# Optimization experiments

Hardware: AMD Instinct MI355X
Metric: run time of the kernel (lower is better)

Reference implementation:

```python
import jax, jax.numpy as jnp
import numpy as np
import math

B_, T_, C_ = 4, 1024, 1024
N_HEAD = 16
INT_D = 64
ALPHA = 1.000001  # sparsity_alpha
N_ITER = 50       # entmax_bisect default iteration count


def _entmax_bisect_impl(X):
    # alpha-entmax over last axis via bisection (entmax package algorithm)
    d = X.shape[-1]
    power = 1.0 / (ALPHA - 1.0)
    Xa = X * (ALPHA - 1.0)
    max_val = jnp.max(Xa, axis=-1, keepdims=True)
    tau_lo = max_val - 1.0                      # gp(1) = 1**power
    tau_hi = max_val - (1.0 / d) ** power       # gp(1/d)
    dm = tau_hi - tau_lo
    p0 = jnp.power(jnp.maximum(Xa - tau_lo, 0.0), power)

    def body(i, carry):
        tau_lo, dm, _ = carry
        dm = dm * 0.5
        tau_m = tau_lo + dm
        p_m = jnp.power(jnp.maximum(Xa - tau_m, 0.0), power)
        f_m = jnp.sum(p_m, axis=-1, keepdims=True) - 1.0
        tau_lo = jnp.where(f_m >= 0, tau_m, tau_lo)
        return (tau_lo, dm, p_m)

    _, _, p_m = jax.lax.fori_loop(0, N_ITER, body, (tau_lo, dm, p0))
    # ensure_sum_one=True
    return p_m / jnp.sum(p_m, axis=-1, keepdims=True)


@jax.custom_vjp
def entmax_bisect(X):
    return _entmax_bisect_impl(X)


def _entmax_fwd(X):
    Y = _entmax_bisect_impl(X)
    return Y, Y


def _entmax_bwd(Y, dY):
    # analytic entmax backward (matches entmax package custom Function)
    gppr = jnp.where(Y > 0, jnp.power(Y, 2.0 - ALPHA), 0.0)
    dX = dY * gppr
    q = jnp.sum(dX, axis=-1, keepdims=True) / jnp.sum(gppr, axis=-1, keepdims=True)
    return (dX - q * gppr,)


entmax_bisect.defvjp(_entmax_fwd, _entmax_bwd)


def setup_inputs() -> dict:
    key = jax.random.key(0)
    ks = jax.random.split(key, 5)
    x = jax.random.normal(ks[0], (B_, T_, C_), jnp.float32)
    W_attn = jax.random.normal(ks[1], (3 * C_, C_), jnp.float32) * 0.02
    W_proj = jax.random.normal(ks[2], (C_, C_), jnp.float32) * 0.02
    Wq_int = jax.random.normal(ks[3], (INT_D, C_), jnp.float32) / math.sqrt(C_)
    Wk_int = jax.random.normal(ks[4], (INT_D, C_), jnp.float32) / math.sqrt(C_)
    int_bias = jnp.ones((1,), jnp.float32) * 5.0  # sparse_attention_int_bias
    return {"x": x, "W_attn": W_attn, "W_proj": W_proj,
            "Wq_int": Wq_int, "Wk_int": Wk_int, "int_bias": int_bias}


def reference(x, W_attn, W_proj, Wq_int, Wk_int, int_bias):
    B, T, C = x.shape
    hd = C // N_HEAD
    # qkv projection (bias=False)
    qkv = x @ W_attn.T                       # (B,T,3C)
    q, k, v = jnp.split(qkv, 3, axis=-1)
    q = q.reshape(B, T, N_HEAD, hd).transpose(0, 2, 1, 3)  # (B,H,T,hd)
    k = k.reshape(B, T, N_HEAD, hd).transpose(0, 2, 1, 3)
    v = v.reshape(B, T, N_HEAD, hd).transpose(0, 2, 1, 3)
    # interaction (gating) projections
    q_int = x @ Wq_int.T                     # (B,T,Di)
    k_int = x @ Wk_int.T
    p_raw = (jnp.einsum('btd,bsd->bts', q_int, k_int) / math.sqrt(INT_D)
             + int_bias[0])[:, None, :, :, None]          # (B,1,T,T,1)
    p_raw = jnp.concatenate([p_raw, jnp.zeros_like(p_raw)], axis=-1)  # (B,1,T,T,2)
    p_int = entmax_bisect(p_raw.astype(jnp.float32))[..., 0]          # (B,1,T,T)
    row = jnp.arange(T)[:, None]
    col = jnp.arange(T)[None, :]
    # bias_int = strict lower triangle; fill 1 where bias_int == 0 (col >= row)
    p_int = jnp.where(col < row, p_int, 1.0)
    cumprobs = jnp.cumprod(p_int, axis=-2)               # over query dim
    attn_mask = jnp.log(cumprobs + 1e-40)                # training-mode epsilon
    attn_mask = jnp.where(col <= row, attn_mask, -jnp.inf)  # causal fill
    # scaled dot-product attention with additive float mask
    scores = jnp.einsum('bhtd,bhsd->bhts', q, k) / math.sqrt(hd) + attn_mask
    probs = jax.nn.softmax(scores, axis=-1)
    y = jnp.einsum('bhts,bhsd->bhtd', probs, v)
    y = y.transpose(0, 2, 1, 3).reshape(B, T, C)
    y = y @ W_proj.T
    return y, cumprobs, attn_mask
```

## Files before the change

kernel.cpp:

```cpp
#include <hip/hip_runtime.h>
#include <cstdint>

#define B_ 4
#define T_ 1024
#define C_ 1024
#define H_ 16
#define HD_ 64
#define DI_ 64
#define NSEG 8

#define NEG_INF (-__builtin_huge_valf())
#define MASK_NEG (-1.0e38f)

typedef __attribute__((ext_vector_type(8))) short short8;
typedef __attribute__((ext_vector_type(4))) float f32x4;

__device__ __forceinline__ unsigned int bf16_rtn(float f) {
  const unsigned int u = __float_as_uint(f);
  return (u + 0x7FFFu + ((u >> 16) & 1u)) >> 16;
}

__global__ __launch_bounds__(256) void split_bf16(const float* __restrict__ in,
                                                  unsigned short* __restrict__ hi,
                                                  unsigned short* __restrict__ lo,
                                                  int n8) {
  const int idx = blockIdx.x * 256 + threadIdx.x;
  if (idx >= n8) return;
  const float4 a = ((const float4*)in)[idx * 2];
  const float4 b = ((const float4*)in)[idx * 2 + 1];
  const float v[8] = {a.x, a.y, a.z, a.w, b.x, b.y, b.z, b.w};
  short8 hv, lv;
#pragma unroll
  for (int j = 0; j < 8; ++j) {
    const unsigned int hb = bf16_rtn(v[j]);
    const float fh = __uint_as_float(hb << 16);
    hv[j] = (short)hb;
    lv[j] = (short)bf16_rtn(v[j] - fh);
  }
  *(short8*)(hi + (size_t)idx * 8) = hv;
  *(short8*)(lo + (size_t)idx * 8) = lv;
}

#define GLDS(ldsoff_bytes, gsrc_ptr)                                                \
  __builtin_amdgcn_global_load_lds(                                                 \
      (const __attribute__((address_space(1))) unsigned int*)(gsrc_ptr),            \
      (__attribute__((address_space(3))) unsigned int*)(ldsc + (ldsoff_bytes)),     \
      16, 0, 0)

__global__ __launch_bounds__(256) void gemm_mfma3(const unsigned short* __restrict__ Ah,
                                                  const unsigned short* __restrict__ Al,
                                                  const unsigned short* __restrict__ Bh,
                                                  const unsigned short* __restrict__ Bl,
                                                  float* __restrict__ Cm,
                                                  int N, int K) {
  __shared__ __align__(16) unsigned short lds[16384];
  char* ldsc = (char*)&lds[0];
  const int tid = threadIdx.x;
  const int w = tid >> 6, l = tid & 63;
  const int bm = blockIdx.x * 128, bn = blockIdx.y * 128;

  const int rr = tid >> 2;
  const int kbyte = (tid & 3) << 4;
  const int kbs = kbyte ^ (((tid >> 3) & 3) << 4);
  const int kbe = kbs >> 1;
  const unsigned short* gAh0 = Ah + (size_t)(bm + rr) * K + kbe;
  const unsigned short* gAh1 = Ah + (size_t)(bm + rr + 64) * K + kbe;
  const unsigned short* gAl0 = Al + (size_t)(bm + rr) * K + kbe;
  const unsigned short* gAl1 = Al + (size_t)(bm + rr + 64) * K + kbe;
  const unsigned short* gBh0 = Bh + (size_t)(bn + rr) * K + kbe;
  const unsigned short* gBh1 = Bh + (size_t)(bn + rr + 64) * K + kbe;
  const unsigned short* gBl0 = Bl + (size_t)(bn + rr) * K + kbe;
  const unsigned short* gBl1 = Bl + (size_t)(bn + rr + 64) * K + kbe;
  const int woff = w << 10;

  const int lmod = l & 15, lqd = l >> 4;
  const int rdswz = (lqd << 4) ^ (((lmod >> 1) & 3) << 4);
  const int arow0 = ((w * 32 + lmod) << 6) + rdswz;
  const int arow1 = ((w * 32 + 16 + lmod) << 6) + rdswz;

  f32x4 acc[2][8];
#pragma unroll
  for (int i = 0; i < 2; ++i)
#pragma unroll
    for (int j = 0; j < 8; ++j) acc[i][j] = (f32x4){0.f, 0.f, 0.f, 0.f};

  for (int k0 = 0; k0 < K; k0 += 32) {
    __syncthreads();
    GLDS(0 + woff, gAh0 + k0);
    GLDS(4096 + woff, gAh1 + k0);
    GLDS(8192 + woff, gAl0 + k0);
    GLDS(12288 + woff, gAl1 + k0);
    GLDS(16384 + woff, gBh0 + k0);
    GLDS(20480 + woff, gBh1 + k0);
    GLDS(24576 + woff, gBl0 + k0);
    GLDS(28672 + woff, gBl1 + k0);
    __syncthreads();

    const short8 ah0 = *(const short8*)(ldsc + arow0);
    const short8 ah1 = *(const short8*)(ldsc + arow1);
    const short8 al0 = *(const short8*)(ldsc + 8192 + arow0);
    const short8 al1 = *(const short8*)(ldsc + 8192 + arow1);
    short8 bh[8], bl[8];
#pragma unroll
    for (int j = 0; j < 8; ++j) {
      const int boff = ((j * 16 + lmod) << 6) + rdswz;
      bh[j] = *(const short8*)(ldsc + 16384 + boff);
      bl[j] = *(const short8*)(ldsc + 24576 + boff);
    }
#pragma unroll
    for (int j = 0; j < 8; ++j) {
      acc[0][j] = __builtin_amdgcn_mfma_f32_16x16x32_bf16(ah0, bh[j], acc[0][j], 0, 0, 0);
      acc[0][j] = __builtin_amdgcn_mfma_f32_16x16x32_bf16(al0, bh[j], acc[0][j], 0, 0, 0);
      acc[0][j] = __builtin_amdgcn_mfma_f32_16x16x32_bf16(ah0, bl[j], acc[0][j], 0, 0, 0);
      acc[1][j] = __builtin_amdgcn_mfma_f32_16x16x32_bf16(ah1, bh[j], acc[1][j], 0, 0, 0);
      acc[1][j] = __builtin_amdgcn_mfma_f32_16x16x32_bf16(al1, bh[j], acc[1][j], 0, 0, 0);
      acc[1][j] = __builtin_amdgcn_mfma_f32_16x16x32_bf16(ah1, bl[j], acc[1][j], 0, 0, 0);
    }
  }
#pragma unroll
  for (int i = 0; i < 2; ++i) {
    const int rowb = bm + w * 32 + i * 16 + lqd * 4;
#pragma unroll
    for (int j = 0; j < 8; ++j) {
      const int col = bn + j * 16 + lmod;
#pragma unroll
      for (int reg = 0; reg < 4; ++reg)
        Cm[(size_t)(rowb + reg) * N + col] = acc[i][j][reg];
    }
  }
}

__global__ __launch_bounds__(256) void gemm_qkv(const unsigned short* __restrict__ Ah,
                                                const unsigned short* __restrict__ Al,
                                                const unsigned short* __restrict__ Bh,
                                                const unsigned short* __restrict__ Bl,
                                                unsigned short* __restrict__ qh,
                                                unsigned short* __restrict__ ql,
                                                unsigned short* __restrict__ kh,
                                                unsigned short* __restrict__ kl,
                                                unsigned short* __restrict__ vth,
                                                unsigned short* __restrict__ vtl,
                                                int K) {
  __shared__ __align__(16) unsigned short lds[16384];
  char* ldsc = (char*)&lds[0];
  const int tid = threadIdx.x;
  const int w = tid >> 6, l = tid & 63;
  const int bm = blockIdx.x * 128, bn = blockIdx.y * 128;

  const int rr = tid >> 2;
  const int kbyte = (tid & 3) << 4;
  const int kbs = kbyte ^ (((tid >> 3) & 3) << 4);
  const int kbe = kbs >> 1;
  const unsigned short* gAh0 = Ah + (size_t)(bm + rr) * K + kbe;
  const unsigned short* gAh1 = Ah + (size_t)(bm + rr + 64) * K + kbe;
  const unsigned short* gAl0 = Al + (size_t)(bm + rr) * K + kbe;
  const unsigned short* gAl1 = Al + (size_t)(bm + rr + 64) * K + kbe;
  const unsigned short* gBh0 = Bh + (size_t)(bn + rr) * K + kbe;
  const unsigned short* gBh1 = Bh + (size_t)(bn + rr + 64) * K + kbe;
  const unsigned short* gBl0 = Bl + (size_t)(bn + rr) * K + kbe;
  const unsigned short* gBl1 = Bl + (size_t)(bn + rr + 64) * K + kbe;
  const int woff = w << 10;

  const int lmod = l & 15, lqd = l >> 4;
  const int rdswz = (lqd << 4) ^ (((lmod >> 1) & 3) << 4);
  const int arow0 = ((w * 32 + lmod) << 6) + rdswz;
  const int arow1 = ((w * 32 + 16 + lmod) << 6) + rdswz;

  f32x4 acc[2][8];
#pragma unroll
  for (int i = 0; i < 2; ++i)
#pragma unroll
    for (int j = 0; j < 8; ++j) acc[i][j] = (f32x4){0.f, 0.f, 0.f, 0.f};

  for (int k0 = 0; k0 < K; k0 += 32) {
    __syncthreads();
    GLDS(0 + woff, gAh0 + k0);
    GLDS(4096 + woff, gAh1 + k0);
    GLDS(8192 + woff, gAl0 + k0);
    GLDS(12288 + woff, gAl1 + k0);
    GLDS(16384 + woff, gBh0 + k0);
    GLDS(20480 + woff, gBh1 + k0);
    GLDS(24576 + woff, gBl0 + k0);
    GLDS(28672 + woff, gBl1 + k0);
    __syncthreads();

    const short8 ah0 = *(const short8*)(ldsc + arow0);
    const short8 ah1 = *(const short8*)(ldsc + arow1);
    const short8 al0 = *(const short8*)(ldsc + 8192 + arow0);
    const short8 al1 = *(const short8*)(ldsc + 8192 + arow1);
    short8 bh[8], bl[8];
#pragma unroll
    for (int j = 0; j < 8; ++j) {
      const int boff = ((j * 16 + lmod) << 6) + rdswz;
      bh[j] = *(const short8*)(ldsc + 16384 + boff);
      bl[j] = *(const short8*)(ldsc + 24576 + boff);
    }
#pragma unroll
    for (int j = 0; j < 8; ++j) {
      acc[0][j] = __builtin_amdgcn_mfma_f32_16x16x32_bf16(ah0, bh[j], acc[0][j], 0, 0, 0);
      acc[0][j] = __builtin_amdgcn_mfma_f32_16x16x32_bf16(al0, bh[j], acc[0][j], 0, 0, 0);
      acc[0][j] = __builtin_amdgcn_mfma_f32_16x16x32_bf16(ah0, bl[j], acc[0][j], 0, 0, 0);
      acc[1][j] = __builtin_amdgcn_mfma_f32_16x16x32_bf16(ah1, bh[j], acc[1][j], 0, 0, 0);
      acc[1][j] = __builtin_amdgcn_mfma_f32_16x16x32_bf16(al1, bh[j], acc[1][j], 0, 0, 0);
      acc[1][j] = __builtin_amdgcn_mfma_f32_16x16x32_bf16(ah1, bl[j], acc[1][j], 0, 0, 0);
    }
  }

  const int part = bn >> 10;
  const int cb = bn & 1023;
#pragma unroll
  for (int i = 0; i < 2; ++i) {
    const int rowb = bm + w * 32 + i * 16 + lqd * 4;
#pragma unroll
    for (int j = 0; j < 8; ++j) {
      const int col = cb + j * 16 + lmod;
#pragma unroll
      for (int reg = 0; reg < 4; ++reg) {
        const float v = acc[i][j][reg];
        const unsigned int hb = bf16_rtn(v);
        const unsigned short lb =
            (unsigned short)bf16_rtn(v - __uint_as_float(hb << 16));
        const int row = rowb + reg;
        if (part == 0) {
          qh[(size_t)row * C_ + col] = (unsigned short)hb;
          ql[(size_t)row * C_ + col] = lb;
        } else if (part == 1) {
          kh[(size_t)row * C_ + col] = (unsigned short)hb;
          kl[(size_t)row * C_ + col] = lb;
        } else {
          const int bb = row >> 10, tt = row & 1023;
          const int hh = col >> 6, dd = col & 63;
          const size_t a = ((size_t)(bb * H_ + hh) * HD_ + dd) * T_ + tt;
          vth[a] = (unsigned short)hb;
          vtl[a] = lb;
        }
      }
    }
  }
}

__global__ __launch_bounds__(256) void qk_int_kernel(const float* __restrict__ x,
                                                     const float* __restrict__ Wq,
                                                     const float* __restrict__ Wk,
                                                     float* __restrict__ qint,
                                                     float* __restrict__ kint) {
  __shared__ __align__(16) float xs[16][64];
  __shared__ __align__(16) float ws[128][68];
  const int tid = threadIdx.x;
  const int m0 = blockIdx.x * 16;
  const int r = tid >> 4, cl = tid & 15;
  float acc[8];
#pragma unroll
  for (int j = 0; j < 8; ++j) acc[j] = 0.0f;

  for (int k0 = 0; k0 < C_; k0 += 64) {
    __syncthreads();
    {
      const int xr = tid >> 4, xc = (tid & 15) << 2;
      *(float4*)&xs[xr][xc] = *(const float4*)(x + (size_t)(m0 + xr) * C_ + k0 + xc);
    }
    {
      const int wr = tid >> 1, off = (tid & 1) << 5;
      const float* wsrc = (wr < 64) ? (Wq + (size_t)wr * C_ + k0 + off)
                                    : (Wk + (size_t)(wr - 64) * C_ + k0 + off);
#pragma unroll
      for (int u = 0; u < 8; ++u)
        *(float4*)&ws[wr][off + u * 4] = *(const float4*)(wsrc + u * 4);
    }
    __syncthreads();
#pragma unroll 4
    for (int k = 0; k < 64; k += 4) {
      const float4 xv = *(const float4*)&xs[r][k];
#pragma unroll
      for (int j = 0; j < 8; ++j) {
        const float4 wv = *(const float4*)&ws[cl + (j << 4)][k];
        acc[j] = fmaf(xv.x, wv.x, acc[j]);
        acc[j] = fmaf(xv.y, wv.y, acc[j]);
        acc[j] = fmaf(xv.z, wv.z, acc[j]);
        acc[j] = fmaf(xv.w, wv.w, acc[j]);
      }
    }
  }
#pragma unroll
  for (int j = 0; j < 8; ++j) {
    const int c = cl + (j << 4);
    if (c < 64) qint[(size_t)(m0 + r) * DI_ + c] = acc[j];
    else        kint[(size_t)(m0 + r) * DI_ + (c - 64)] = acc[j];
  }
}

__device__ __forceinline__ float pow_1e6(float b) {
  const float u = b - 1.0f;
  if (u < -1.2e-4f) return 0.0f;
  const float lg = u * fmaf(u, fmaf(u, 0.33333333f, -0.5f), 1.0f);
  return __expf(1.0e6f * lg);
}

__device__ float entmax_p0(float s) {
  const float AM1 = (float)(1.000001 - 1.0);
  const float xa = s * AM1;
  const float mx = fmaxf(xa, 0.0f);
  float tau = mx - 1.0f;
  float dm = 0x1p-17f;
  float pm0 = 0.0f, pm1 = 0.0f;
#pragma unroll 1
  for (int i = 0; i < 16; ++i) {
    dm *= 0.5f;
    const float tm = tau + dm;
    pm0 = pow_1e6(fmaxf(xa - tm, 0.0f));
    pm1 = pow_1e6(fmaxf(0.0f - tm, 0.0f));
    const bool frozen = (tm == tau);
    if (pm0 + pm1 - 1.0f >= 0.0f) tau = tm;
    if (frozen) break;
  }
  return pm0 / (pm0 + pm1);
}

__global__ __launch_bounds__(256) void pint_kernel(const float* __restrict__ qint,
                                                   const float* __restrict__ kint,
                                                   const float* __restrict__ bias,
                                                   float* __restrict__ p) {
  __shared__ __align__(16) float qs[16][68];
  __shared__ __align__(16) float ks[16][68];
  const int b = blockIdx.y;
  const int tile = blockIdx.x;
  int trr = (int)((sqrtf(8.0f * (float)tile + 1.0f) - 1.0f) * 0.5f);
  while ((trr + 1) * (trr + 2) / 2 <= tile) ++trr;
  while (trr * (trr + 1) / 2 > tile) --trr;
  const int tcc = tile - trr * (trr + 1) / 2;
  const int t0 = trr * 16, s0 = tcc * 16;
  const int tid = threadIdx.x;

  const int lrow = tid >> 4, ld4 = (tid & 15) << 2;
  *(float4*)&qs[lrow][ld4] = *(const float4*)(qint + ((size_t)(b * T_ + t0 + lrow)) * DI_ + ld4);
  *(float4*)&ks[lrow][ld4] = *(const float4*)(kint + ((size_t)(b * T_ + s0 + lrow)) * DI_ + ld4);
  __syncthreads();

  const int tl = tid >> 4, sl = tid & 15;
  const int t = t0 + tl, s = s0 + sl;
  if (s < t) {
    float acc = 0.0f;
#pragma unroll
    for (int d = 0; d < DI_; d += 4) {
      const float4 q4 = *(const float4*)&qs[tl][d];
      const float4 k4 = *(const float4*)&ks[sl][d];
      acc = fmaf(q4.x, k4.x, acc); acc = fmaf(q4.y, k4.y, acc);
      acc = fmaf(q4.z, k4.z, acc); acc = fmaf(q4.w, k4.w, acc);
    }
    const float sv = acc * 0.125f + bias[0];
    p[((size_t)b * T_ + t) * T_ + s] = entmax_p0(sv);
  }
}

__global__ __launch_bounds__(256) void scan_seg(const float* __restrict__ p,
                                                float* __restrict__ seg) {
  const int s = blockIdx.x * 256 + threadIdx.x;
  const int sg = blockIdx.y, b = blockIdx.z;
  const int t0 = sg * (T_ / NSEG);
  float r = 1.0f;
  for (int t = t0; t < t0 + T_ / NSEG; ++t) {
    if (s < t) r *= p[((size_t)b * T_ + t) * T_ + s];
  }
  seg[((size_t)b * NSEG + sg) * T_ + s] = r;
}

__global__ __launch_bounds__(256) void scan_write(const float* __restrict__ p,
                                                  const float* __restrict__ seg,
                                                  float* __restrict__ cumprobs,
                                                  float* __restrict__ mask) {
  const int s = blockIdx.x * 256 + threadIdx.x;
  const int sg = blockIdx.y, b = blockIdx.z;
  const int t0 = sg * (T_ / NSEG);
  float r = 1.0f;
  for (int k = 0; k < sg; ++k) r *= seg[((size_t)b * NSEG + k) * T_ + s];
  for (int t = t0; t < t0 + T_ / NSEG; ++t) {
    if (s < t) r *= p[((size_t)b * T_ + t) * T_ + s];
    const size_t off = ((size_t)b * T_ + t) * T_ + s;
    cumprobs[off] = r;
    mask[off] = (s <= t) ? logf(r + 1e-40f) : MASK_NEG;
  }
}

__global__ __launch_bounds__(256) void attn_mfma(const unsigned short* __restrict__ qh,
                                                 const unsigned short* __restrict__ ql,
                                                 const unsigned short* __restrict__ kh,
                                                 const unsigned short* __restrict__ kl,
                                                 const unsigned short* __restrict__ vth,
                                                 const unsigned short* __restrict__ vtl,
                                                 const float* __restrict__ mask,
                                                 float* __restrict__ y1) {
  __shared__ __align__(16) unsigned short KV[16384];
  __shared__ __align__(16) unsigned short PhL[64 * 72];
  __shared__ __align__(16) unsigned short PlL[64 * 72];
  __shared__ float pmaxL[4][64];
  __shared__ float psumL[4][64];
  __shared__ float scaleL[64];
  __shared__ float linvL[64];

  const int b = blockIdx.z, h = blockIdx.y, t0 = blockIdx.x * 64;
  const int tid = threadIdx.x;
  const int w = tid >> 6, l = tid & 63;
  const int lmod = l & 15, lqd = l >> 4;
  char* ldsc = (char*)&KV[0];

  const int srow = l >> 3;
  const int sslot = (l & 7) ^ (srow & 7);

  short8 qfh[4][2], qfl[4][2];
#pragma unroll
  for (int jj = 0; jj < 4; ++jj)
#pragma unroll
    for (int kk = 0; kk < 2; ++kk) {
      const size_t qi = ((size_t)(b * T_ + t0 + jj * 16 + lmod)) * C_ + h * HD_ + kk * 32 + lqd * 8;
      qfh[jj][kk] = *(const short8*)(qh + qi);
      qfl[jj][kk] = *(const short8*)(ql + qi);
    }

  float mreg[4], lreg[4];
#pragma unroll
  for (int jj = 0; jj < 4; ++jj) { mreg[jj] = NEG_INF; lreg[jj] = 0.0f; }
  f32x4 pacc[4];
#pragma unroll
  for (int dd = 0; dd < 4; ++dd) pacc[dd] = (f32x4){0.f, 0.f, 0.f, 0.f};

  for (int s0 = 0; s0 <= t0; s0 += 64) {
    __syncthreads();
#pragma unroll
    for (int c = 0; c < 2; ++c) {
      const int row = w * 16 + c * 8 + srow;
      const size_t kidx = (size_t)(b * T_ + s0 + row) * C_ + h * HD_ + sslot * 8;
      const size_t vidx = ((size_t)(b * H_ + h) * HD_ + row) * T_ + s0 + sslot * 8;
      const int ldst = (w * 16 + c * 8) * 128;
      GLDS(0 + ldst, kh + kidx);
      GLDS(8192 + ldst, kl + kidx);
      GLDS(16384 + ldst, vth + vidx);
      GLDS(24576 + ldst, vtl + vidx);
    }
    float4 mv[4];
#pragma unroll
    for (int jj = 0; jj < 4; ++jj)
      mv[jj] = *(const float4*)(mask + ((size_t)(b * T_ + t0 + jj * 16 + lmod)) * T_ + s0 + w * 16 + lqd * 4);
    __syncthreads();

    f32x4 sa[4];
#pragma unroll
    for (int jj = 0; jj < 4; ++jj) sa[jj] = (f32x4){0.f, 0.f, 0.f, 0.f};
#pragma unroll
    for (int kk = 0; kk < 2; ++kk) {
      const int koff = (w * 16 + lmod) * 128 + (((kk * 4 + lqd) ^ (lmod & 7)) << 4);
      const short8 kAh = *(const short8*)(ldsc + koff);
      const short8 kAl = *(const short8*)(ldsc + 8192 + koff);
#pragma unroll
      for (int jj = 0; jj < 4; ++jj) {
        sa[jj] = __builtin_amdgcn_mfma_f32_16x16x32_bf16(kAh, qfh[jj][kk], sa[jj], 0, 0, 0);
        sa[jj] = __builtin_amdgcn_mfma_f32_16x16x32_bf16(kAl, qfh[jj][kk], sa[jj], 0, 0, 0);
        sa[jj] = __builtin_amdgcn_mfma_f32_16x16x32_bf16(kAh, qfl[jj][kk], sa[jj], 0, 0, 0);
      }
    }

    float sv[4][4];
#pragma unroll
    for (int jj = 0; jj < 4; ++jj) {
      sv[jj][0] = sa[jj][0] * 0.125f + mv[jj].x;
      sv[jj][1] = sa[jj][1] * 0.125f + mv[jj].y;
      sv[jj][2] = sa[jj][2] * 0.125f + mv[jj].z;
      sv[jj][3] = sa[jj][3] * 0.125f + mv[jj].w;
      float v = fmaxf(fmaxf(sv[jj][0], sv[jj][1]), fmaxf(sv[jj][2], sv[jj][3]));
      v = fmaxf(v, __shfl_xor(v, 16));
      v = fmaxf(v, __shfl_xor(v, 32));
      if (lqd == 0) pmaxL[w][jj * 16 + lmod] = v;
    }
    __syncthreads();

    float sc[4];
#pragma unroll
    for (int jj = 0; jj < 4; ++jj) {
      const int t = jj * 16 + lmod;
      const float cm = fmaxf(fmaxf(pmaxL[0][t], pmaxL[1][t]), fmaxf(pmaxL[2][t], pmaxL[3][t]));
      const float mn = fmaxf(mreg[jj], cm);
      sc[jj] = expf(mreg[jj] - mn);
      mreg[jj] = mn;
      const float p0 = expf(sv[jj][0] - mn);
      const float p1 = expf(sv[jj][1] - mn);
      const float p2 = expf(sv[jj][2] - mn);
      const float p3 = expf(sv[jj][3] - mn);
      float ss = (p0 + p1) + (p2 + p3);
      ss += __shfl_xor(ss, 16);
      ss += __shfl_xor(ss, 32);
      if (lqd == 0) psumL[w][t] = ss;
      const unsigned int h0 = bf16_rtn(p0), h1 = bf16_rtn(p1);
      const unsigned int h2 = bf16_rtn(p2), h3 = bf16_rtn(p3);
      const unsigned int l0 = bf16_rtn(p0 - __uint_as_float(h0 << 16));
      const unsigned int l1 = bf16_rtn(p1 - __uint_as_float(h1 << 16));
      const unsigned int l2 = bf16_rtn(p2 - __uint_as_float(h2 << 16));
      const unsigned int l3 = bf16_rtn(p3 - __uint_as_float(h3 << 16));
      uint2 wh, wl;
      wh.x = h0 | (h1 << 16); wh.y = h2 | (h3 << 16);
      wl.x = l0 | (l1 << 16); wl.y = l2 | (l3 << 16);
      const int po = t * 72 + w * 16 + lqd * 4;
      *(uint2*)&PhL[po] = wh;
      *(uint2*)&PlL[po] = wl;
    }
    if (w == 0 && lqd == 0) {
#pragma unroll
      for (int jj = 0; jj < 4; ++jj) scaleL[jj * 16 + lmod] = sc[jj];
    }
    __syncthreads();

#pragma unroll
    for (int jj = 0; jj < 4; ++jj) {
      const int t = jj * 16 + lmod;
      lreg[jj] = lreg[jj] * sc[jj] + ((psumL[0][t] + psumL[1][t]) + (psumL[2][t] + psumL[3][t]));
    }
    float rs[4];
#pragma unroll
    for (int r = 0; r < 4; ++r) rs[r] = scaleL[w * 16 + lqd * 4 + r];
#pragma unroll
    for (int dd = 0; dd < 4; ++dd)
#pragma unroll
      for (int r = 0; r < 4; ++r) pacc[dd][r] *= rs[r];

    short8 pah[2], pal[2];
#pragma unroll
    for (int kk = 0; kk < 2; ++kk) {
      const int po = (w * 16 + lmod) * 144 + kk * 64 + lqd * 16;
      pah[kk] = *(const short8*)((const char*)&PhL[0] + po);
      pal[kk] = *(const short8*)((const char*)&PlL[0] + po);
    }
#pragma unroll
    for (int dd = 0; dd < 4; ++dd) {
#pragma unroll
      for (int kk = 0; kk < 2; ++kk) {
        const int voff = (dd * 16 + lmod) * 128 + (((kk * 4 + lqd) ^ (lmod & 7)) << 4);
        const short8 vfh = *(const short8*)(ldsc + 16384 + voff);
        const short8 vfl = *(const short8*)(ldsc + 24576 + voff);
        pacc[dd] = __builtin_amdgcn_mfma_f32_16x16x32_bf16(pah[kk], vfh, pacc[dd], 0, 0, 0);
        pacc[dd] = __builtin_amdgcn_mfma_f32_16x16x32_bf16(pal[kk], vfh, pacc[dd], 0, 0, 0);
        pacc[dd] = __builtin_amdgcn_mfma_f32_16x16x32_bf16(pah[kk], vfl, pacc[dd], 0, 0, 0);
      }
    }
  }

  if (w == 0 && lqd == 0) {
#pragma unroll
    for (int jj = 0; jj < 4; ++jj) linvL[jj * 16 + lmod] = 1.0f / lreg[jj];
  }
  __syncthreads();
  float rs[4];
#pragma unroll
  for (int r = 0; r < 4; ++r) rs[r] = linvL[w * 16 + lqd * 4 + r];
#pragma unroll
  for (int dd = 0; dd < 4; ++dd)
#pragma unroll
    for (int r = 0; r < 4; ++r) {
      const int t = t0 + w * 16 + lqd * 4 + r;
      y1[((size_t)(b * T_ + t)) * C_ + h * HD_ + dd * 16 + lmod] = pacc[dd][r] * rs[r];
    }
}

extern "C" void kernel_launch(void* const* d_in, const int* in_sizes, int n_in,
                              void* d_out, int out_size, void* d_ws, size_t ws_size,
                              hipStream_t stream) {
  const float* x      = (const float*)d_in[0];
  const float* W_attn = (const float*)d_in[1];
  const float* W_proj = (const float*)d_in[2];
  const float* Wq     = (const float*)d_in[3];
  const float* Wk     = (const float*)d_in[4];
  const float* bias   = (const float*)d_in[5];
  float* ws  = (float*)d_ws;
  float* out = (float*)d_out;
  (void)ws_size; (void)n_in; (void)in_sizes; (void)out_size;

  const int M = B_ * T_;
  const size_t MC = (size_t)M * C_;
  unsigned short* qh  = (unsigned short*)ws;
  unsigned short* ql  = qh + MC;
  unsigned short* kh  = ql + MC;
  unsigned short* kl  = kh + MC;
  unsigned short* vth = kl + MC;
  unsigned short* vtl = vth + MC;
  float* qint = ws + (size_t)M * 3 * C_;
  float* kint = qint + (size_t)M * DI_;
  float* p    = kint + (size_t)M * DI_;
  float* seg  = p + (size_t)B_ * T_ * T_;
  unsigned short* xh  = (unsigned short*)(seg + (size_t)B_ * NSEG * T_);
  unsigned short* xl  = xh + MC;
  unsigned short* wph = (unsigned short*)(xl + MC);
  unsigned short* wpl = wph + (size_t)C_ * C_;
  unsigned short* wah = (unsigned short*)p;
  unsigned short* wal = wah + (size_t)3 * C_ * C_;
  float* y1 = p;
  unsigned short* y1h = qh;
  unsigned short* y1l = y1h + MC;

  float* y_out    = out;
  float* cumprobs = out + MC;
  float* maskp    = cumprobs + (size_t)B_ * T_ * T_;

  const dim3 blk(256);
  split_bf16<<<dim3((M * C_ / 8) / 256), blk, 0, stream>>>(x, xh, xl, M * C_ / 8);
  split_bf16<<<dim3((3 * C_ * C_ / 8) / 256), blk, 0, stream>>>(W_attn, wah, wal, 3 * C_ * C_ / 8);
  split_bf16<<<dim3((C_ * C_ / 8) / 256), blk, 0, stream>>>(W_proj, wph, wpl, C_ * C_ / 8);
  qk_int_kernel<<<dim3(M / 16), blk, 0, stream>>>(x, Wq, Wk, qint, kint);
  gemm_qkv<<<dim3(M / 128, (3 * C_) / 128), blk, 0, stream>>>(xh, xl, wah, wal,
                                                              qh, ql, kh, kl, vth, vtl, C_);
  pint_kernel<<<dim3(2080, B_), blk, 0, stream>>>(qint, kint, bias, p);
  scan_seg<<<dim3(T_ / 256, NSEG, B_), blk, 0, stream>>>(p, seg);
  scan_write<<<dim3(T_ / 256, NSEG, B_), blk, 0, stream>>>(p, seg, cumprobs, maskp);
  attn_mfma<<<dim3(T_ / 64, H_, B_), blk, 0, stream>>>(qh, ql, kh, kl, vth, vtl, maskp, y1);
  split_bf16<<<dim3((M * C_ / 8) / 256), blk, 0, stream>>>(y1, y1h, y1l, M * C_ / 8);
  gemm_mfma3<<<dim3(M / 128, C_ / 128), blk, 0, stream>>>(y1h, y1l, wph, wpl, y_out, C_, C_);
}
```

Measured before the change: 577.2 us.

## Share K/V tiles across two query groups in 512-thread attention blocks

```diff
diff --git a/kernel.cpp b/kernel.cpp
--- a/kernel.cpp
+++ b/kernel.cpp
@@ -381,7 +381,7 @@
   }
 }
 
-__global__ __launch_bounds__(256) void attn_mfma(const unsigned short* __restrict__ qh,
+__global__ __launch_bounds__(512) void attn_mfma(const unsigned short* __restrict__ qh,
                                                  const unsigned short* __restrict__ ql,
                                                  const unsigned short* __restrict__ kh,
                                                  const unsigned short* __restrict__ kl,
@@ -390,28 +390,31 @@
                                                  const float* __restrict__ mask,
                                                  float* __restrict__ y1) {
   __shared__ __align__(16) unsigned short KV[16384];
-  __shared__ __align__(16) unsigned short PhL[64 * 72];
-  __shared__ __align__(16) unsigned short PlL[64 * 72];
-  __shared__ float pmaxL[4][64];
-  __shared__ float psumL[4][64];
-  __shared__ float scaleL[64];
-  __shared__ float linvL[64];
-
-  const int b = blockIdx.z, h = blockIdx.y, t0 = blockIdx.x * 64;
+  __shared__ __align__(16) unsigned short Pb[2][8192];
+  __shared__ float pmaxL[2][4][64];
+  __shared__ float psumL[2][4][64];
+  __shared__ float scaleL[2][64];
+  __shared__ float linvL[2][64];
+
+  const int b = blockIdx.z, h = blockIdx.y, t0 = blockIdx.x * 128;
   const int tid = threadIdx.x;
   const int w = tid >> 6, l = tid & 63;
+  const int g = w >> 2, wl = w & 3;
+  const int tg0 = t0 + g * 64;
   const int lmod = l & 15, lqd = l >> 4;
   char* ldsc = (char*)&KV[0];
-
-  const int srow = l >> 3;
-  const int sslot = (l & 7) ^ (srow & 7);
+  char* pbase = (char*)&Pb[g][0];
+
+  const int srow = w * 8 + (l >> 3);
+  const int sslot = (l & 7) ^ (l >> 3);
+  const int ldst = w * 1024;
 
   short8 qfh[4][2], qfl[4][2];
 #pragma unroll
   for (int jj = 0; jj < 4; ++jj)
 #pragma unroll
     for (int kk = 0; kk < 2; ++kk) {
-      const size_t qi = ((size_t)(b * T_ + t0 + jj * 16 + lmod)) * C_ + h * HD_ + kk * 32 + lqd * 8;
+      const size_t qi = ((size_t)(b * T_ + tg0 + jj * 16 + lmod)) * C_ + h * HD_ + kk * 32 + lqd * 8;
       qfh[jj][kk] = *(const short8*)(qh + qi);
       qfl[jj][kk] = *(const short8*)(ql + qi);
     }
@@ -423,137 +426,145 @@
 #pragma unroll
   for (int dd = 0; dd < 4; ++dd) pacc[dd] = (f32x4){0.f, 0.f, 0.f, 0.f};
 
-  for (int s0 = 0; s0 <= t0; s0 += 64) {
-    __syncthreads();
-#pragma unroll
-    for (int c = 0; c < 2; ++c) {
-      const int row = w * 16 + c * 8 + srow;
-      const size_t kidx = (size_t)(b * T_ + s0 + row) * C_ + h * HD_ + sslot * 8;
-      const size_t vidx = ((size_t)(b * H_ + h) * HD_ + row) * T_ + s0 + sslot * 8;
-      const int ldst = (w * 16 + c * 8) * 128;
+  const int send = t0 + 64;
+  for (int s0 = 0; s0 <= send; s0 += 64) {
+    const bool active = (s0 <= tg0 + 63);
+    __syncthreads();
+    {
+      const size_t kidx = (size_t)(b * T_ + s0 + srow) * C_ + h * HD_ + sslot * 8;
+      const size_t vidx = ((size_t)(b * H_ + h) * HD_ + srow) * T_ + s0 + sslot * 8;
       GLDS(0 + ldst, kh + kidx);
       GLDS(8192 + ldst, kl + kidx);
       GLDS(16384 + ldst, vth + vidx);
       GLDS(24576 + ldst, vtl + vidx);
     }
     float4 mv[4];
-#pragma unroll
-    for (int jj = 0; jj < 4; ++jj)
-      mv[jj] = *(const float4*)(mask + ((size_t)(b * T_ + t0 + jj * 16 + lmod)) * T_ + s0 + w * 16 + lqd * 4);
-    __syncthreads();
-
-    f32x4 sa[4];
-#pragma unroll
-    for (int jj = 0; jj < 4; ++jj) sa[jj] = (f32x4){0.f, 0.f, 0.f, 0.f};
-#pragma unroll
-    for (int kk = 0; kk < 2; ++kk) {
-      const int koff = (w * 16 + lmod) * 128 + (((kk * 4 + lqd) ^ (lmod & 7)) << 4);
-      const short8 kAh = *(const short8*)(ldsc + koff);
-      const short8 kAl = *(const short8*)(ldsc + 8192 + koff);
+    if (active) {
+#pragma unroll
+      for (int jj = 0; jj < 4; ++jj)
+        mv[jj] = *(const float4*)(mask + ((size_t)(b * T_ + tg0 + jj * 16 + lmod)) * T_ + s0 + wl * 16 + lqd * 4);
+    }
+    __syncthreads();
+
+    float sv[4][4];
+    if (active) {
+      f32x4 sa[4];
+#pragma unroll
+      for (int jj = 0; jj < 4; ++jj) sa[jj] = (f32x4){0.f, 0.f, 0.f, 0.f};
+#pragma unroll
+      for (int kk = 0; kk < 2; ++kk) {
+        const int koff = (wl * 16 + lmod) * 128 + (((kk * 4 + lqd) ^ (lmod & 7)) << 4);
+        const short8 kAh = *(const short8*)(ldsc + koff);
+        const short8 kAl = *(const short8*)(ldsc + 8192 + koff);
+#pragma unroll
+        for (int jj = 0; jj < 4; ++jj) {
+          sa[jj] = __builtin_amdgcn_mfma_f32_16x16x32_bf16(kAh, qfh[jj][kk], sa[jj], 0, 0, 0);
+          sa[jj] = __builtin_amdgcn_mfma_f32_16x16x32_bf16(kAl, qfh[jj][kk], sa[jj], 0, 0, 0);
+          sa[jj] = __builtin_amdgcn_mfma_f32_16x16x32_bf16(kAh, qfl[jj][kk], sa[jj], 0, 0, 0);
+        }
+      }
 #pragma unroll
       for (int jj = 0; jj < 4; ++jj) {
-        sa[jj] = __builtin_amdgcn_mfma_f32_16x16x32_bf16(kAh, qfh[jj][kk], sa[jj], 0, 0, 0);
-        sa[jj] = __builtin_amdgcn_mfma_f32_16x16x32_bf16(kAl, qfh[jj][kk], sa[jj], 0, 0, 0);
-        sa[jj] = __builtin_amdgcn_mfma_f32_16x16x32_bf16(kAh, qfl[jj][kk], sa[jj], 0, 0, 0);
-      }
-    }
-
-    float sv[4][4];
-#pragma unroll
-    for (int jj = 0; jj < 4; ++jj) {
-      sv[jj][0] = sa[jj][0] * 0.125f + mv[jj].x;
-      sv[jj][1] = sa[jj][1] * 0.125f + mv[jj].y;
-      sv[jj][2] = sa[jj][2] * 0.125f + mv[jj].z;
-      sv[jj][3] = sa[jj][3] * 0.125f + mv[jj].w;
-      float v = fmaxf(fmaxf(sv[jj][0], sv[jj][1]), fmaxf(sv[jj][2], sv[jj][3]));
-      v = fmaxf(v, __shfl_xor(v, 16));
-      v = fmaxf(v, __shfl_xor(v, 32));
-      if (lqd == 0) pmaxL[w][jj * 16 + lmod] = v;
+        sv[jj][0] = sa[jj][0] * 0.125f + mv[jj].x;
+        sv[jj][1] = sa[jj][1] * 0.125f + mv[jj].y;
+        sv[jj][2] = sa[jj][2] * 0.125f + mv[jj].z;
+        sv[jj][3] = sa[jj][3] * 0.125f + mv[jj].w;
+        float v = fmaxf(fmaxf(sv[jj][0], sv[jj][1]), fmaxf(sv[jj][2], sv[jj][3]));
+        v = fmaxf(v, __shfl_xor(v, 16));
+        v = fmaxf(v, __shfl_xor(v, 32));
+        if (lqd == 0) pmaxL[g][wl][jj * 16 + lmod] = v;
+      }
     }
     __syncthreads();
 
     float sc[4];
-#pragma unroll
-    for (int jj = 0; jj < 4; ++jj) {
-      const int t = jj * 16 + lmod;
-      const float cm = fmaxf(fmaxf(pmaxL[0][t], pmaxL[1][t]), fmaxf(pmaxL[2][t], pmaxL[3][t]));
-      const float mn = fmaxf(mreg[jj], cm);
-      sc[jj] = expf(mreg[jj] - mn);
-      mreg[jj] = mn;
-      const float p0 = expf(sv[jj][0] - mn);
-      const float p1 = expf(sv[jj][1] - mn);
-      const float p2 = expf(sv[jj][2] - mn);
-      const float p3 = expf(sv[jj][3] - mn);
-      float ss = (p0 + p1) + (p2 + p3);
-      ss += __shfl_xor(ss, 16);
-      ss += __shfl_xor(ss, 32);
-      if (lqd == 0) psumL[w][t] = ss;
-      const unsigned int h0 = bf16_rtn(p0), h1 = bf16_rtn(p1);
-      const unsigned int h2 = bf16_rtn(p2), h3 = bf16_rtn(p3);
-      const unsigned int l0 = bf16_rtn(p0 - __uint_as_float(h0 << 16));
-      const unsigned int l1 = bf16_rtn(p1 - __uint_as_float(h1 << 16));
-      const unsigned int l2 = bf16_rtn(p2 - __uint_as_float(h2 << 16));
-      const unsigned int l3 = bf16_rtn(p3 - __uint_as_float(h3 << 16));
-      uint2 wh, wl;
-      wh.x = h0 | (h1 << 16); wh.y = h2 | (h3 << 16);
-      wl.x = l0 | (l1 << 16); wl.y = l2 | (l3 << 16);
-      const int po = t * 72 + w * 16 + lqd * 4;
-      *(uint2*)&PhL[po] = wh;
-      *(uint2*)&PlL[po] = wl;
-    }
-    if (w == 0 && lqd == 0) {
-#pragma unroll
-      for (int jj = 0; jj < 4; ++jj) scaleL[jj * 16 + lmod] = sc[jj];
-    }
-    __syncthreads();
-
-#pragma unroll
-    for (int jj = 0; jj < 4; ++jj) {
-      const int t = jj * 16 + lmod;
-      lreg[jj] = lreg[jj] * sc[jj] + ((psumL[0][t] + psumL[1][t]) + (psumL[2][t] + psumL[3][t]));
-    }
-    float rs[4];
-#pragma unroll
-    for (int r = 0; r < 4; ++r) rs[r] = scaleL[w * 16 + lqd * 4 + r];
-#pragma unroll
-    for (int dd = 0; dd < 4; ++dd)
-#pragma unroll
-      for (int r = 0; r < 4; ++r) pacc[dd][r] *= rs[r];
-
-    short8 pah[2], pal[2];
-#pragma unroll
-    for (int kk = 0; kk < 2; ++kk) {
-      const int po = (w * 16 + lmod) * 144 + kk * 64 + lqd * 16;
-      pah[kk] = *(const short8*)((const char*)&PhL[0] + po);
-      pal[kk] = *(const short8*)((const char*)&PlL[0] + po);
-    }
-#pragma unroll
-    for (int dd = 0; dd < 4; ++dd) {
+    if (active) {
+#pragma unroll
+      for (int jj = 0; jj < 4; ++jj) {
+        const int t = jj * 16 + lmod;
+        const float cm = fmaxf(fmaxf(pmaxL[g][0][t], pmaxL[g][1][t]),
+                               fmaxf(pmaxL[g][2][t], pmaxL[g][3][t]));
+        const float mn = fmaxf(mreg[jj], cm);
+        sc[jj] = expf(mreg[jj] - mn);
+        mreg[jj] = mn;
+        const float p0 = expf(sv[jj][0] - mn);
+        const float p1 = expf(sv[jj][1] - mn);
+        const float p2 = expf(sv[jj][2] - mn);
+        const float p3 = expf(sv[jj][3] - mn);
+        float ss = (p0 + p1) + (p2 + p3);
+        ss += __shfl_xor(ss, 16);
+        ss += __shfl_xor(ss, 32);
+        if (lqd == 0) psumL[g][wl][t] = ss;
+        const unsigned int h0 = bf16_rtn(p0), h1 = bf16_rtn(p1);
+        const unsigned int h2 = bf16_rtn(p2), h3 = bf16_rtn(p3);
+        const unsigned int l0 = bf16_rtn(p0 - __uint_as_float(h0 << 16));
+        const unsigned int l1 = bf16_rtn(p1 - __uint_as_float(h1 << 16));
+        const unsigned int l2 = bf16_rtn(p2 - __uint_as_float(h2 << 16));
+        const unsigned int l3 = bf16_rtn(p3 - __uint_as_float(h3 << 16));
+        uint2 wh, wlo;
+        wh.x = h0 | (h1 << 16); wh.y = h2 | (h3 << 16);
+        wlo.x = l0 | (l1 << 16); wlo.y = l2 | (l3 << 16);
+        const int po = (t * 128 + wl * 32 + lqd * 8) ^ ((t & 7) << 4);
+        *(uint2*)(pbase + po) = wh;
+        *(uint2*)(pbase + 8192 + po) = wlo;
+      }
+      if (wl == 0 && lqd == 0) {
+#pragma unroll
+        for (int jj = 0; jj < 4; ++jj) scaleL[g][jj * 16 + lmod] = sc[jj];
+      }
+    }
+    __syncthreads();
+
+    if (active) {
+#pragma unroll
+      for (int jj = 0; jj < 4; ++jj) {
+        const int t = jj * 16 + lmod;
+        lreg[jj] = lreg[jj] * sc[jj] +
+                   ((psumL[g][0][t] + psumL[g][1][t]) + (psumL[g][2][t] + psumL[g][3][t]));
+      }
+      float rs[4];
+#pragma unroll
+      for (int r = 0; r < 4; ++r) rs[r] = scaleL[g][wl * 16 + lqd * 4 + r];
+#pragma unroll
+      for (int dd = 0; dd < 4; ++dd)
+#pragma unroll
+        for (int r = 0; r < 4; ++r) pacc[dd][r] *= rs[r];
+
+      short8 pah[2], pal[2];
 #pragma unroll
       for (int kk = 0; kk < 2; ++kk) {
-        const int voff = (dd * 16 + lmod) * 128 + (((kk * 4 + lqd) ^ (lmod & 7)) << 4);
-        const short8 vfh = *(const short8*)(ldsc + 16384 + voff);
-        const short8 vfl = *(const short8*)(ldsc + 24576 + voff);
-        pacc[dd] = __builtin_amdgcn_mfma_f32_16x16x32_bf16(pah[kk], vfh, pacc[dd], 0, 0, 0);
-        pacc[dd] = __builtin_amdgcn_mfma_f32_16x16x32_bf16(pal[kk], vfh, pacc[dd], 0, 0, 0);
-        pacc[dd] = __builtin_amdgcn_mfma_f32_16x16x32_bf16(pah[kk], vfl, pacc[dd], 0, 0, 0);
-      }
-    }
-  }
-
-  if (w == 0 && lqd == 0) {
-#pragma unroll
-    for (int jj = 0; jj < 4; ++jj) linvL[jj * 16 + lmod] = 1.0f / lreg[jj];
+        const int po = ((wl * 16 + lmod) * 128 + kk * 64 + lqd * 16) ^ ((lmod & 7) << 4);
+        pah[kk] = *(const short8*)(pbase + po);
+        pal[kk] = *(const short8*)(pbase + 8192 + po);
+      }
+#pragma unroll
+      for (int dd = 0; dd < 4; ++dd) {
+#pragma unroll
+        for (int kk = 0; kk < 2; ++kk) {
+          const int voff = (dd * 16 + lmod) * 128 + (((kk * 4 + lqd) ^ (lmod & 7)) << 4);
+          const short8 vfh = *(const short8*)(ldsc + 16384 + voff);
+          const short8 vfl = *(const short8*)(ldsc + 24576 + voff);
+          pacc[dd] = __builtin_amdgcn_mfma_f32_16x16x32_bf16(pah[kk], vfh, pacc[dd], 0, 0, 0);
+          pacc[dd] = __builtin_amdgcn_mfma_f32_16x16x32_bf16(pal[kk], vfh, pacc[dd], 0, 0, 0);
+          pacc[dd] = __builtin_amdgcn_mfma_f32_16x16x32_bf16(pah[kk], vfl, pacc[dd], 0, 0, 0);
+        }
+      }
+    }
+  }
+
+  if (wl == 0 && lqd == 0) {
+#pragma unroll
+    for (int jj = 0; jj < 4; ++jj) linvL[g][jj * 16 + lmod] = 1.0f / lreg[jj];
   }
   __syncthreads();
   float rs[4];
 #pragma unroll
-  for (int r = 0; r < 4; ++r) rs[r] = linvL[w * 16 + lqd * 4 + r];
+  for (int r = 0; r < 4; ++r) rs[r] = linvL[g][wl * 16 + lqd * 4 + r];
 #pragma unroll
   for (int dd = 0; dd < 4; ++dd)
 #pragma unroll
     for (int r = 0; r < 4; ++r) {
-      const int t = t0 + w * 16 + lqd * 4 + r;
+      const int t = tg0 + wl * 16 + lqd * 4 + r;
       y1[((size_t)(b * T_ + t)) * C_ + h * HD_ + dd * 16 + lmod] = pacc[dd][r] * rs[r];
     }
 }
@@ -607,7 +618,7 @@
   pint_kernel<<<dim3(2080, B_), blk, 0, stream>>>(qint, kint, bias, p);
   scan_seg<<<dim3(T_ / 256, NSEG, B_), blk, 0, stream>>>(p, seg);
   scan_write<<<dim3(T_ / 256, NSEG, B_), blk, 0, stream>>>(p, seg, cumprobs, maskp);
-  attn_mfma<<<dim3(T_ / 64, H_, B_), blk, 0, stream>>>(qh, ql, kh, kl, vth, vtl, maskp, y1);
+  attn_mfma<<<dim3(T_ / 128, H_, B_), dim3(512), 0, stream>>>(qh, ql, kh, kl, vth, vtl, maskp, y1);
   split_bf16<<<dim3((M * C_ / 8) / 256), blk, 0, stream>>>(y1, y1h, y1l, M * C_ / 8);
   gemm_mfma3<<<dim3(M / 128, C_ / 128), blk, 0, stream>>>(y1h, y1l, wph, wpl, y_out, C_, C_);
 }
```

Result: no change. 580.4 us (+0.6%).
